# Kernel optimization log

Hardware: AMD Instinct MI355X
Metric: run time of the kernel (lower is better)

The kernel has to match this reference:

```python
import jax, jax.numpy as jnp
import numpy as np

N, K, C_S, C_Z, C_G, N_RBF = 1024, 16, 256, 128, 16, 64
EPS = 1e-8


def _ln(x, g, b, eps=1e-5):
    m = x.mean(-1, keepdims=True)
    v = jnp.mean((x - m) ** 2, -1, keepdims=True)
    return (x - m) * jax.lax.rsqrt(v + eps) * g + b


def _rbf(D, D_count=N_RBF, D_min=0.0, D_max=20.0):
    mu = jnp.linspace(D_min, D_max, D_count, dtype=D.dtype)
    sigma = (D_max - D_min) / D_count
    return jnp.exp(-(((D[..., None] - mu) / sigma) ** 2))


def setup_inputs() -> dict:
    key = jax.random.key(0)
    ks = jax.random.split(key, 20)
    node_features = jax.random.normal(ks[0], (N, C_S), jnp.float32)
    trans = jax.random.normal(ks[1], (N, 3), jnp.float32) * 5.0  # CA translations, Angstrom-ish
    edge_features = jax.random.normal(ks[2], (N * K, C_Z), jnp.float32)
    # sparse graph laid out as K neighbors per node: dst = node i repeated K times
    src = jax.random.randint(ks[3], (N * K,), 0, N)
    dst = jnp.repeat(jnp.arange(N), K)
    edge_index = jnp.stack([src, dst]).astype(jnp.int64)
    batch = jnp.zeros((N,), jnp.int64)
    res_mask = jnp.ones((N,), bool)
    w = lambda k, i, o: jax.random.normal(k, (i, o), jnp.float32) * 0.02
    return {
        "node_features": node_features, "trans": trans, "edge_features": edge_features,
        "ln_g": jnp.ones((C_Z,), jnp.float32), "ln_b": jnp.zeros((C_Z,), jnp.float32),
        "Wl": w(ks[4], C_S, C_G), "bl": jnp.zeros((C_G,), jnp.float32),
        "Wr": w(ks[5], C_S, C_G), "br": jnp.zeros((C_G,), jnp.float32),
        "Wep": w(ks[6], C_Z, C_Z), "bep": jnp.zeros((C_Z,), jnp.float32),
        "Weg": w(ks[7], C_Z, C_Z), "beg": jnp.zeros((C_Z,), jnp.float32),
        "Wdg": w(ks[8], C_G * C_G, C_Z), "bdg": jnp.zeros((C_Z,), jnp.float32),
        "Wdp": w(ks[9], N_RBF, C_Z), "bdp": jnp.zeros((C_Z,), jnp.float32),
        "lno_g": jnp.ones((C_Z,), jnp.float32), "lno_b": jnp.zeros((C_Z,), jnp.float32),
        "Wout": w(ks[10], C_Z, C_Z), "bout": jnp.zeros((C_Z,), jnp.float32),
        "Wog": w(ks[11], C_Z, C_Z), "bog": jnp.zeros((C_Z,), jnp.float32),
        "edge_index": edge_index, "batch": batch, "res_mask": res_mask,
    }


def reference(node_features, trans, edge_features, ln_g, ln_b, Wl, bl, Wr, br,
              Wep, bep, Weg, beg, Wdg, bdg, Wdp, bdp, lno_g, lno_b, Wout, bout,
              Wog, bog, edge_index, batch, res_mask):
    n = node_features.shape[0]
    src = edge_index[0].reshape(n, K)              # neighbor indices per node [N,K]
    # sparse -> kNN: edges are grouped K per destination node
    knn_feats = edge_features.reshape(n, K, C_Z)
    knn_mask = res_mask[src] & res_mask[:, None]   # [N,K]
    z = _ln(knn_feats, ln_g, ln_b)
    # outer-product node gating
    nl = node_features @ Wl + bl                   # [N,c_g]
    nr = node_features @ Wr + br
    a = nl[src]                                    # [N,K,c_g]
    b = nr[src]
    edge3 = a[:, :, None, :, None] * b[:, None, :, None, :]   # [N,K,K,c_g,c_g]
    gate3 = edge3.reshape(n, K, K, C_G * C_G) @ Wdg + bdg     # [N,K,K,c_z]
    # RBF distance features among the K neighbors of each node
    t = trans[src]                                 # [N,K,3]
    d = jnp.linalg.norm(t[:, :, None, :] - t[:, None, :, :] + EPS, axis=-1)  # [N,K,K]
    df = _rbf(d) @ Wdp + bdp                       # [N,K,K,c_z]
    m2 = (knn_mask[:, :, None] & knn_mask[:, None, :]).astype(df.dtype)
    e3 = jax.nn.sigmoid(gate3) * df * m2[..., None]
    # gated edge projection
    e2 = jax.nn.sigmoid(z @ Weg + beg) * (z @ Wep + bep)      # [N,K,c_z]
    # triangle matmul: per channel c, [K,K] @ [K]
    upd = jnp.einsum('njkc,nkc->njc', e3, e2)                 # [N,K,c_z]
    upd = _ln(upd, lno_g, lno_b) @ Wout + bout
    upd = upd * jax.nn.sigmoid(z @ Wog + bog)
    # kNN -> sparse scatter back (masked)
    out = (upd * knn_mask[..., None].astype(upd.dtype)).reshape(n * K, C_Z)
    return out
```

## Files before the change

### kernel.cpp

```cpp
#include <hip/hip_runtime.h>
#include <math.h>

#define KNN  16
#define CZ   128
#define CG   16
#define CS   256
#define NN   1024

typedef __attribute__((ext_vector_type(8))) _Float16 half8;
typedef __attribute__((ext_vector_type(4))) _Float16 half4;
typedef __attribute__((ext_vector_type(2))) _Float16 half2v;
typedef __attribute__((ext_vector_type(4))) float f4_t;

#define MFMA16x32(A, B, C) __builtin_amdgcn_mfma_f32_16x16x32_f16((A), (B), (C), 0, 0, 0)
#define MFMA16x16(A, B, C) __builtin_amdgcn_mfma_f32_16x16x16f16((A), (B), (C), 0, 0, 0)

union U8 { half2v h[4]; half8 v; };
union U4 { half2v h[2]; half4 v; };

__device__ __forceinline__ half2v pk2(float x, float y) {
    auto t = __builtin_amdgcn_cvt_pkrtz(x, y);
    half2v r;
    __builtin_memcpy(&r, &t, 4);
    return r;
}
__device__ __forceinline__ float sig_(float x) {
    return __builtin_amdgcn_rcpf(1.0f + __expf(-x));
}

__global__ __launch_bounds__(256) void prep_kernel(
    const float* __restrict__ Wdp, const float* __restrict__ Wdg,
    const float* __restrict__ Wout, const float* __restrict__ Wep,
    const float* __restrict__ Weg, const float* __restrict__ Wog,
    _Float16* __restrict__ pk,
    const float* __restrict__ nf,
    const float* __restrict__ Wl, const float* __restrict__ bl,
    const float* __restrict__ Wr, const float* __restrict__ br,
    float* __restrict__ nlo, float* __restrict__ nro) {
    __shared__ float pl[4][16], pr[4][16];
    int b = blockIdx.x, tid = threadIdx.x;
    if (b < 416) {
        int gid = b * 256 + tid;
        float val;
        if (gid >= 8192 && gid < 40960) {
            int o = gid - 8192;
            int i = o & 3, l = (o >> 2) & 63, ct = (o >> 8) & 7, q = o >> 11;
            int row = (4 * (l >> 4) + i) * 16 + q;
            int col = ct * 16 + (l & 15);
            val = Wdg[row * CZ + col];
        } else {
            const float* srcw;
            int o;
            if (gid < 8192)        { srcw = Wdp;  o = gid; }
            else if (gid < 57344)  { srcw = Wout; o = gid - 40960; }
            else if (gid < 73728)  { srcw = Wep;  o = gid - 57344; }
            else if (gid < 90112)  { srcw = Weg;  o = gid - 73728; }
            else                   { srcw = Wog;  o = gid - 90112; }
            int t = o & 7, l = (o >> 3) & 63, ct = (o >> 9) & 7, s = o >> 12;
            int row = s * 32 + (l >> 4) * 8 + t;
            int col = ct * 16 + (l & 15);
            val = srcw[row * CZ + col];
        }
        pk[gid] = (_Float16)val;
    } else {
        int n = b - 416;
        int wv = tid >> 6, lane = tid & 63;
        int p = lane & 15, sub = lane >> 4;
        int base = wv * 64 + sub * 16;
        const float* rw = nf + n * CS + base;
        const float* wlp = Wl + base * CG + p;
        const float* wrp = Wr + base * CG + p;
        float accl = 0.0f, accr = 0.0f;
        #pragma unroll
        for (int i = 0; i < 16; ++i) {
            float v = rw[i];
            accl += v * wlp[i * CG];
            accr += v * wrp[i * CG];
        }
        accl += __shfl_xor(accl, 16); accl += __shfl_xor(accl, 32);
        accr += __shfl_xor(accr, 16); accr += __shfl_xor(accr, 32);
        if (lane < 16) { pl[wv][lane] = accl; pr[wv][lane] = accr; }
        __syncthreads();
        if (tid < 16) {
            nlo[n * CG + tid] = pl[0][tid] + pl[1][tid] + pl[2][tid] + pl[3][tid] + bl[tid];
        } else if (tid < 32) {
            int p2 = tid - 16;
            nro[n * CG + p2] = pr[0][p2] + pr[1][p2] + pr[2][p2] + pr[3][p2] + br[p2];
        }
    }
}

__global__ __launch_bounds__(256) void main_kernel(
    const float* __restrict__ trans, const float* __restrict__ ef,
    const float* __restrict__ lng, const float* __restrict__ lnb,
    const float* __restrict__ nl, const float* __restrict__ nr,
    const float* __restrict__ bep, const float* __restrict__ beg,
    const float* __restrict__ bog,
    const _Float16* __restrict__ Wepp, const _Float16* __restrict__ Wegp,
    const _Float16* __restrict__ Wogp,
    const _Float16* __restrict__ Wdg2, const float* __restrict__ bdg,
    const _Float16* __restrict__ Wdpp, const float* __restrict__ bdp,
    const float* __restrict__ lnog, const float* __restrict__ lnob,
    const _Float16* __restrict__ Woutp, const float* __restrict__ bout,
    const int* __restrict__ src, const int* __restrict__ resmask,
    float* __restrict__ out) {
    __shared__ _Float16 s_zu[16 * 136];
    __shared__ float s_t[64];
    __shared__ float s_km[16];
    __shared__ int   s_src[16];
    __shared__ float s_a[256];
    __shared__ float s_b[16 * 20];
    __shared__ _Float16 s_T[4 * 2048];
    __shared__ _Float16 s_fr[8 * 64 * 8];
    __shared__ _Float16 s_part[16 * CZ * 4];

    int n = blockIdx.x, tid = threadIdx.x;
    if (tid < 16) {
        int sv = src[n * KNN + tid];
        s_src[tid] = sv;
        s_km[tid] = (resmask[sv] != 0 && resmask[n] != 0) ? 1.0f : 0.0f;
        s_t[tid * 4 + 0] = trans[sv * 3 + 0];
        s_t[tid * 4 + 1] = trans[sv * 3 + 1];
        s_t[tid * 4 + 2] = trans[sv * 3 + 2];
    }
    __syncthreads();
    {
        int j = tid >> 4, p = tid & 15;
        int sv = s_src[j];
        s_a[j * 16 + p] = nl[sv * CG + p];
        s_b[j * 20 + p] = nr[sv * CG + p];
    }
    {
        int r = tid >> 4, seg = tid & 15;
        const float* row = ef + ((size_t)n * KNN + r) * CZ + seg * 8;
        f4_t x0 = *(const f4_t*)row;
        f4_t x1 = *(const f4_t*)(row + 4);
        float s = x0.x + x0.y + x0.z + x0.w + x1.x + x1.y + x1.z + x1.w;
        float q = x0.x * x0.x + x0.y * x0.y + x0.z * x0.z + x0.w * x0.w
                + x1.x * x1.x + x1.y * x1.y + x1.z * x1.z + x1.w * x1.w;
        #pragma unroll
        for (int m = 1; m < 16; m <<= 1) { s += __shfl_xor(s, m); q += __shfl_xor(q, m); }
        float mean = s * (1.0f / CZ);
        float var  = q * (1.0f / CZ) - mean * mean;
        float rs   = __builtin_amdgcn_rsqf(var + 1e-5f);
        int col = seg * 8;
        f4_t g0 = *(const f4_t*)(lng + col), g1 = *(const f4_t*)(lng + col + 4);
        f4_t b0 = *(const f4_t*)(lnb + col), b1 = *(const f4_t*)(lnb + col + 4);
        U8 zu;
        zu.h[0] = pk2((x0.x - mean) * rs * g0.x + b0.x, (x0.y - mean) * rs * g0.y + b0.y);
        zu.h[1] = pk2((x0.z - mean) * rs * g0.z + b0.z, (x0.w - mean) * rs * g0.w + b0.w);
        zu.h[2] = pk2((x1.x - mean) * rs * g1.x + b1.x, (x1.y - mean) * rs * g1.y + b1.y);
        zu.h[3] = pk2((x1.z - mean) * rs * g1.z + b1.z, (x1.w - mean) * rs * g1.w + b1.w);
        *(half8*)&s_zu[r * 136 + col] = zu.v;
    }
    __syncthreads();

    int wv = tid >> 6, lane = tid & 63, l15 = lane & 15, quad = lane >> 4;

    half8 Az[4];
    #pragma unroll
    for (int st = 0; st < 4; ++st)
        Az[st] = *(const half8*)&s_zu[l15 * 136 + st * 32 + quad * 8];
    f4_t e2f[2], ggf[2];
    #pragma unroll
    for (int cc = 0; cc < 2; ++cc) {
        int ct = wv * 2 + cc;
        int c = ct * 16 + l15;
        float vep = bep[c], veg = beg[c], vog = bog[c];
        f4_t aep = {vep, vep, vep, vep};
        f4_t aeg = {veg, veg, veg, veg};
        f4_t aog = {vog, vog, vog, vog};
        #pragma unroll
        for (int st = 0; st < 4; ++st) {
            int off = ((st * 8 + ct) * 64 + lane) * 8;
            half8 wep_ = *(const half8*)(Wepp + off);
            half8 weg_ = *(const half8*)(Wegp + off);
            half8 wog_ = *(const half8*)(Wogp + off);
            aep = MFMA16x32(Az[st], wep_, aep);
            aeg = MFMA16x32(Az[st], weg_, aeg);
            aog = MFMA16x32(Az[st], wog_, aog);
        }
        #pragma unroll
        for (int rr = 0; rr < 4; ++rr) {
            e2f[cc][rr] = sig_(aeg[rr]) * aep[rr] * s_km[quad * 4 + rr];
            ggf[cc][rr] = sig_(aog[rr]);
        }
    }
    __syncthreads();

    {
        U8 g;
        g.h[0] = pk2(ggf[0][0], ggf[0][1]);
        g.h[1] = pk2(ggf[0][2], ggf[0][3]);
        g.h[2] = pk2(ggf[1][0], ggf[1][1]);
        g.h[3] = pk2(ggf[1][2], ggf[1][3]);
        *(half8*)&s_zu[tid * 8] = g.v;
    }

    half8 Bdp_[2][2];
    #pragma unroll
    for (int st = 0; st < 2; ++st)
        #pragma unroll
        for (int cc = 0; cc < 2; ++cc)
            Bdp_[st][cc] = *(const half8*)(Wdpp + ((st * 8 + wv * 2 + cc) * 64 + lane) * 8);

    float bdgv[2], bdpv[2];
    #pragma unroll
    for (int cc = 0; cc < 2; ++cc) {
        int c = (wv * 2 + cc) * 16 + l15;
        bdgv[cc] = bdg[c];
        bdpv[cc] = bdp[c];
    }

    half4 Aa, Ab;
    {
        f4_t av = *(const f4_t*)&s_a[l15 * 16 + 4 * quad];
        U4 u; u.h[0] = pk2(av.x, av.y); u.h[1] = pk2(av.z, av.w);
        Aa = u.v;
        f4_t bv = *(const f4_t*)&s_b[l15 * 20 + 4 * quad];
        U4 w; w.h[0] = pk2(bv.x, bv.y); w.h[1] = pk2(bv.z, bv.w);
        Ab = w.v;
    }

    float tkx = s_t[l15 * 4 + 0], tky = s_t[l15 * 4 + 1], tkz = s_t[l15 * 4 + 2];
    const float MUS = 20.0f / 63.0f;
    const float ISG = 1.0f / 0.3125f;
    float rIS[2];
    #pragma unroll
    for (int st = 0; st < 2; ++st)
        rIS[st] = (float)(st * 32 + quad * 8) * (MUS * ISG);

    _Float16* Tw = s_T + wv * 2048;

    for (int Q = 0; Q < 4; ++Q) {
        #pragma unroll
        for (int ctl = 0; ctl < 2; ++ctl) {
            int ct = wv * 2 + ctl;
            #pragma unroll
            for (int qb = 0; qb < 4; ++qb) {
                f4_t tq[4];
                #pragma unroll
                for (int qq = 0; qq < 4; ++qq) {
                    half4 Bw = *(const half4*)(Wdg2 + (((4 * qb + qq) * 8 + ct) * 64 + lane) * 4);
                    f4_t z = {0.f, 0.f, 0.f, 0.f};
                    tq[qq] = MFMA16x16(Aa, Bw, z);
                }
                if (quad == Q) {
                    #pragma unroll
                    for (int rr = 0; rr < 4; ++rr) {
                        U4 u;
                        u.h[0] = pk2(tq[0][rr], tq[1][rr]);
                        u.h[1] = pk2(tq[2][rr], tq[3][rr]);
                        *(half4*)&Tw[((rr * 2 + ctl) * 64 + l15 + 16 * qb) * 4] = u.v;
                    }
                }
            }
        }

        #pragma unroll
        for (int uu = 0; uu < 2; ++uu) {
            int u = wv * 2 + uu;
            int m = u >> 1, st = u & 1;
            int j = 4 * Q + m;
            float dx = s_t[j * 4 + 0] - tkx + 1e-8f;
            float dy = s_t[j * 4 + 1] - tky + 1e-8f;
            float dz = s_t[j * 4 + 2] - tkz + 1e-8f;
            float dI = sqrtf(dx * dx + dy * dy + dz * dz) * ISG;
            float base0 = dI - rIS[st];
            U8 cv;
            #pragma unroll
            for (int tt = 0; tt < 4; ++tt) {
                float u0 = base0 - (float)(2 * tt) * (MUS * ISG);
                float u1 = u0 - (MUS * ISG);
                cv.h[tt] = pk2(__expf(-u0 * u0), __expf(-u1 * u1));
            }
            *(half8*)&s_fr[(u * 64 + lane) * 8] = cv.v;
        }
        __syncthreads();

        for (int m = 0; m < 4; ++m) {
            int j = 4 * Q + m;
            half8 ar0 = *(const half8*)&s_fr[((m * 2 + 0) * 64 + lane) * 8];
            half8 ar1 = *(const half8*)&s_fr[((m * 2 + 1) * 64 + lane) * 8];
            f4_t accd[2], accg[2];
            #pragma unroll
            for (int cc = 0; cc < 2; ++cc) {
                f4_t z = {bdpv[cc], bdpv[cc], bdpv[cc], bdpv[cc]};
                z = MFMA16x32(ar0, Bdp_[0][cc], z);
                z = MFMA16x32(ar1, Bdp_[1][cc], z);
                accd[cc] = z;
                half4 Bt = *(const half4*)&Tw[((m * 2 + cc) * 64 + l15 + 16 * quad) * 4];
                f4_t g = {bdgv[cc], bdgv[cc], bdgv[cc], bdgv[cc]};
                accg[cc] = MFMA16x16(Ab, Bt, g);
            }
            #pragma unroll
            for (int cc = 0; cc < 2; ++cc) {
                float pr = 0.f;
                #pragma unroll
                for (int rr = 0; rr < 4; ++rr)
                    pr += sig_(accg[cc][rr]) * accd[cc][rr] * e2f[cc][rr];
                s_part[(j * CZ + (wv * 2 + cc) * 16 + l15) * 4 + quad] = (_Float16)pr;
            }
        }
        __syncthreads();
    }

    half8 gv = *(const half8*)&s_zu[tid * 8];
    __syncthreads();

    #pragma unroll
    for (int rr2 = 0; rr2 < 4; ++rr2) {
        int rj = wv * 4 + rr2;
        U4 p0, p1;
        p0.v = *(const half4*)&s_part[(rj * CZ + lane) * 4];
        p1.v = *(const half4*)&s_part[(rj * CZ + lane + 64) * 4];
        half2v t0 = p0.h[0] + p0.h[1];
        half2v t1 = p1.h[0] + p1.h[1];
        float x0 = (float)t0[0] + (float)t0[1];
        float x1 = (float)t1[0] + (float)t1[1];
        float sm = x0 + x1, sq = x0 * x0 + x1 * x1;
        #pragma unroll
        for (int m = 1; m < 64; m <<= 1) {
            sm += __shfl_xor(sm, m);
            sq += __shfl_xor(sq, m);
        }
        float mean = sm * (1.0f / CZ);
        float var  = sq * (1.0f / CZ) - mean * mean;
        float rsv  = __builtin_amdgcn_rsqf(var + 1e-5f);
        float h0 = (x0 - mean) * rsv * lnog[lane] + lnob[lane];
        float h1 = (x1 - mean) * rsv * lnog[64 + lane] + lnob[64 + lane];
        s_zu[rj * 136 + lane]      = (_Float16)h0;
        s_zu[rj * 136 + 64 + lane] = (_Float16)h1;
    }
    __syncthreads();

    half8 Aw[4];
    #pragma unroll
    for (int st = 0; st < 4; ++st)
        Aw[st] = *(const half8*)&s_zu[l15 * 136 + st * 32 + quad * 8];
    #pragma unroll
    for (int cc = 0; cc < 2; ++cc) {
        int ct = wv * 2 + cc;
        int c = ct * 16 + l15;
        float bo = bout[c];
        f4_t acc = {bo, bo, bo, bo};
        #pragma unroll
        for (int st = 0; st < 4; ++st) {
            half8 bw = *(const half8*)(Woutp + ((st * 8 + ct) * 64 + lane) * 8);
            acc = MFMA16x32(Aw[st], bw, acc);
        }
        #pragma unroll
        for (int rr = 0; rr < 4; ++rr) {
            int row = quad * 4 + rr;
            size_t oi = (size_t)(n * KNN + row) * CZ + c;
            out[oi] = acc[rr] * (float)gv[cc * 4 + rr] * s_km[row];
        }
    }
}

extern "C" void kernel_launch(void* const* d_in, const int* in_sizes, int n_in,
                              void* d_out, int out_size, void* d_ws, size_t ws_size,
                              hipStream_t stream) {
    const float* node_features = (const float*)d_in[0];
    const float* trans         = (const float*)d_in[1];
    const float* edge_features = (const float*)d_in[2];
    const float* ln_g  = (const float*)d_in[3];
    const float* ln_b  = (const float*)d_in[4];
    const float* Wl    = (const float*)d_in[5];
    const float* bl    = (const float*)d_in[6];
    const float* Wr    = (const float*)d_in[7];
    const float* br    = (const float*)d_in[8];
    const float* Wep   = (const float*)d_in[9];
    const float* bep   = (const float*)d_in[10];
    const float* Weg   = (const float*)d_in[11];
    const float* beg   = (const float*)d_in[12];
    const float* Wdg   = (const float*)d_in[13];
    const float* bdg   = (const float*)d_in[14];
    const float* Wdp   = (const float*)d_in[15];
    const float* bdp   = (const float*)d_in[16];
    const float* lno_g = (const float*)d_in[17];
    const float* lno_b = (const float*)d_in[18];
    const float* Wout  = (const float*)d_in[19];
    const float* bout  = (const float*)d_in[20];
    const float* Wog   = (const float*)d_in[21];
    const float* bog   = (const float*)d_in[22];
    const int* edge_index = (const int*)d_in[23];
    const int* resmask    = (const int*)d_in[25];

    float* ws = (float*)d_ws;
    float* nl = ws;
    float* nr = nl + NN * CG;
    _Float16* pk = (_Float16*)(nr + NN * CG);
    _Float16* Wdpp  = pk;
    _Float16* Wdg2  = pk + 8192;
    _Float16* Woutp = pk + 40960;
    _Float16* Wepp  = pk + 57344;
    _Float16* Wegp  = pk + 73728;
    _Float16* Wogp  = pk + 90112;
    const int* src = edge_index;

    prep_kernel<<<1440, 256, 0, stream>>>(
        Wdp, Wdg, Wout, Wep, Weg, Wog, pk,
        node_features, Wl, bl, Wr, br, nl, nr);
    main_kernel<<<NN, 256, 0, stream>>>(
        trans, edge_features, ln_g, ln_b, nl, nr,
        bep, beg, bog, Wepp, Wegp, Wogp,
        Wdg2, bdg, Wdpp, bdp, lno_g, lno_b,
        Woutp, bout, src, resmask, (float*)d_out);
}
```

Baseline: 150.4 us.

## Double main kernel block to 512 threads, one channel tile per wave

Main kernel now runs 8 waves per block instead of 4, with each wave handling a single 16-channel tile rather than two. The layernorm load, RBF feature generation, triangle partial products and output projection are all re-split across the larger block, and the per-wave shared T buffer is halved. The aim is more parallelism and latency hiding per node at the cost of fewer registers per thread and more threads sharing the same barriers.

```diff
diff --git a/kernel.cpp b/kernel.cpp
--- a/kernel.cpp
+++ b/kernel.cpp
@@ -90,7 +90,7 @@
     }
 }
 
-__global__ __launch_bounds__(256) void main_kernel(
+__global__ __launch_bounds__(512) void main_kernel(
     const float* __restrict__ trans, const float* __restrict__ ef,
     const float* __restrict__ lng, const float* __restrict__ lnb,
     const float* __restrict__ nl, const float* __restrict__ nr,
@@ -110,7 +110,7 @@
     __shared__ int   s_src[16];
     __shared__ float s_a[256];
     __shared__ float s_b[16 * 20];
-    __shared__ _Float16 s_T[4 * 2048];
+    __shared__ _Float16 s_T[8 * 1024];
     __shared__ _Float16 s_fr[8 * 64 * 8];
     __shared__ _Float16 s_part[16 * CZ * 4];
 
@@ -124,48 +124,43 @@
         s_t[tid * 4 + 2] = trans[sv * 3 + 2];
     }
     __syncthreads();
-    {
+    if (tid < 256) {
         int j = tid >> 4, p = tid & 15;
         int sv = s_src[j];
         s_a[j * 16 + p] = nl[sv * CG + p];
         s_b[j * 20 + p] = nr[sv * CG + p];
     }
     {
-        int r = tid >> 4, seg = tid & 15;
-        const float* row = ef + ((size_t)n * KNN + r) * CZ + seg * 8;
-        f4_t x0 = *(const f4_t*)row;
-        f4_t x1 = *(const f4_t*)(row + 4);
-        float s = x0.x + x0.y + x0.z + x0.w + x1.x + x1.y + x1.z + x1.w;
-        float q = x0.x * x0.x + x0.y * x0.y + x0.z * x0.z + x0.w * x0.w
-                + x1.x * x1.x + x1.y * x1.y + x1.z * x1.z + x1.w * x1.w;
-        #pragma unroll
-        for (int m = 1; m < 16; m <<= 1) { s += __shfl_xor(s, m); q += __shfl_xor(q, m); }
+        int r = tid >> 5, seg = tid & 31;
+        int col = seg * 4;
+        const float* row = ef + ((size_t)n * KNN + r) * CZ + col;
+        f4_t x = *(const f4_t*)row;
+        float s = x.x + x.y + x.z + x.w;
+        float q = x.x * x.x + x.y * x.y + x.z * x.z + x.w * x.w;
+        #pragma unroll
+        for (int m = 1; m < 32; m <<= 1) { s += __shfl_xor(s, m); q += __shfl_xor(q, m); }
         float mean = s * (1.0f / CZ);
         float var  = q * (1.0f / CZ) - mean * mean;
         float rs   = __builtin_amdgcn_rsqf(var + 1e-5f);
-        int col = seg * 8;
-        f4_t g0 = *(const f4_t*)(lng + col), g1 = *(const f4_t*)(lng + col + 4);
-        f4_t b0 = *(const f4_t*)(lnb + col), b1 = *(const f4_t*)(lnb + col + 4);
-        U8 zu;
-        zu.h[0] = pk2((x0.x - mean) * rs * g0.x + b0.x, (x0.y - mean) * rs * g0.y + b0.y);
-        zu.h[1] = pk2((x0.z - mean) * rs * g0.z + b0.z, (x0.w - mean) * rs * g0.w + b0.w);
-        zu.h[2] = pk2((x1.x - mean) * rs * g1.x + b1.x, (x1.y - mean) * rs * g1.y + b1.y);
-        zu.h[3] = pk2((x1.z - mean) * rs * g1.z + b1.z, (x1.w - mean) * rs * g1.w + b1.w);
-        *(half8*)&s_zu[r * 136 + col] = zu.v;
+        f4_t g = *(const f4_t*)(lng + col);
+        f4_t bb = *(const f4_t*)(lnb + col);
+        U4 zu;
+        zu.h[0] = pk2((x.x - mean) * rs * g.x + bb.x, (x.y - mean) * rs * g.y + bb.y);
+        zu.h[1] = pk2((x.z - mean) * rs * g.z + bb.z, (x.w - mean) * rs * g.w + bb.w);
+        *(half4*)&s_zu[r * 136 + col] = zu.v;
     }
     __syncthreads();
 
     int wv = tid >> 6, lane = tid & 63, l15 = lane & 15, quad = lane >> 4;
+    int ct = wv;
+    int c = ct * 16 + l15;
 
     half8 Az[4];
     #pragma unroll
     for (int st = 0; st < 4; ++st)
         Az[st] = *(const half8*)&s_zu[l15 * 136 + st * 32 + quad * 8];
-    f4_t e2f[2], ggf[2];
-    #pragma unroll
-    for (int cc = 0; cc < 2; ++cc) {
-        int ct = wv * 2 + cc;
-        int c = ct * 16 + l15;
+    f4_t e2f, ggf;
+    {
         float vep = bep[c], veg = beg[c], vog = bog[c];
         f4_t aep = {vep, vep, vep, vep};
         f4_t aeg = {veg, veg, veg, veg};
@@ -182,35 +177,25 @@
         }
         #pragma unroll
         for (int rr = 0; rr < 4; ++rr) {
-            e2f[cc][rr] = sig_(aeg[rr]) * aep[rr] * s_km[quad * 4 + rr];
-            ggf[cc][rr] = sig_(aog[rr]);
-        }
-    }
-    __syncthreads();
-
-    {
-        U8 g;
-        g.h[0] = pk2(ggf[0][0], ggf[0][1]);
-        g.h[1] = pk2(ggf[0][2], ggf[0][3]);
-        g.h[2] = pk2(ggf[1][0], ggf[1][1]);
-        g.h[3] = pk2(ggf[1][2], ggf[1][3]);
-        *(half8*)&s_zu[tid * 8] = g.v;
-    }
-
-    half8 Bdp_[2][2];
+            e2f[rr] = sig_(aeg[rr]) * aep[rr] * s_km[quad * 4 + rr];
+            ggf[rr] = sig_(aog[rr]);
+        }
+    }
+    __syncthreads();
+
+    {
+        U4 g;
+        g.h[0] = pk2(ggf[0], ggf[1]);
+        g.h[1] = pk2(ggf[2], ggf[3]);
+        *(half4*)&s_zu[tid * 4] = g.v;
+    }
+
+    half8 Bdp_[2];
     #pragma unroll
     for (int st = 0; st < 2; ++st)
-        #pragma unroll
-        for (int cc = 0; cc < 2; ++cc)
-            Bdp_[st][cc] = *(const half8*)(Wdpp + ((st * 8 + wv * 2 + cc) * 64 + lane) * 8);
-
-    float bdgv[2], bdpv[2];
-    #pragma unroll
-    for (int cc = 0; cc < 2; ++cc) {
-        int c = (wv * 2 + cc) * 16 + l15;
-        bdgv[cc] = bdg[c];
-        bdpv[cc] = bdp[c];
-    }
+        Bdp_[st] = *(const half8*)(Wdpp + ((st * 8 + ct) * 64 + lane) * 8);
+
+    float bdgv = bdg[c], bdpv = bdp[c];
 
     half4 Aa, Ab;
     {
@@ -225,48 +210,39 @@
     float tkx = s_t[l15 * 4 + 0], tky = s_t[l15 * 4 + 1], tkz = s_t[l15 * 4 + 2];
     const float MUS = 20.0f / 63.0f;
     const float ISG = 1.0f / 0.3125f;
-    float rIS[2];
-    #pragma unroll
-    for (int st = 0; st < 2; ++st)
-        rIS[st] = (float)(st * 32 + quad * 8) * (MUS * ISG);
-
-    _Float16* Tw = s_T + wv * 2048;
+    int ust = wv & 1;
+    float rISu = (float)(ust * 32 + quad * 8) * (MUS * ISG);
+
+    _Float16* Tw = s_T + wv * 1024;
 
     for (int Q = 0; Q < 4; ++Q) {
         #pragma unroll
-        for (int ctl = 0; ctl < 2; ++ctl) {
-            int ct = wv * 2 + ctl;
+        for (int qb = 0; qb < 4; ++qb) {
+            f4_t tq[4];
             #pragma unroll
-            for (int qb = 0; qb < 4; ++qb) {
-                f4_t tq[4];
+            for (int qq = 0; qq < 4; ++qq) {
+                half4 Bw = *(const half4*)(Wdg2 + (((4 * qb + qq) * 8 + ct) * 64 + lane) * 4);
+                f4_t z = {0.f, 0.f, 0.f, 0.f};
+                tq[qq] = MFMA16x16(Aa, Bw, z);
+            }
+            if (quad == Q) {
                 #pragma unroll
-                for (int qq = 0; qq < 4; ++qq) {
-                    half4 Bw = *(const half4*)(Wdg2 + (((4 * qb + qq) * 8 + ct) * 64 + lane) * 4);
-                    f4_t z = {0.f, 0.f, 0.f, 0.f};
-                    tq[qq] = MFMA16x16(Aa, Bw, z);
-                }
-                if (quad == Q) {
-                    #pragma unroll
-                    for (int rr = 0; rr < 4; ++rr) {
-                        U4 u;
-                        u.h[0] = pk2(tq[0][rr], tq[1][rr]);
-                        u.h[1] = pk2(tq[2][rr], tq[3][rr]);
-                        *(half4*)&Tw[((rr * 2 + ctl) * 64 + l15 + 16 * qb) * 4] = u.v;
-                    }
+                for (int rr = 0; rr < 4; ++rr) {
+                    U4 u;
+                    u.h[0] = pk2(tq[0][rr], tq[1][rr]);
+                    u.h[1] = pk2(tq[2][rr], tq[3][rr]);
+                    *(half4*)&Tw[(rr * 64 + l15 + 16 * qb) * 4] = u.v;
                 }
             }
         }
 
-        #pragma unroll
-        for (int uu = 0; uu < 2; ++uu) {
-            int u = wv * 2 + uu;
-            int m = u >> 1, st = u & 1;
-            int j = 4 * Q + m;
+        {
+            int j = 4 * Q + (wv >> 1);
             float dx = s_t[j * 4 + 0] - tkx + 1e-8f;
             float dy = s_t[j * 4 + 1] - tky + 1e-8f;
             float dz = s_t[j * 4 + 2] - tkz + 1e-8f;
             float dI = sqrtf(dx * dx + dy * dy + dz * dz) * ISG;
-            float base0 = dI - rIS[st];
+            float base0 = dI - rISu;
             U8 cv;
             #pragma unroll
             for (int tt = 0; tt < 4; ++tt) {
@@ -274,7 +250,7 @@
                 float u1 = u0 - (MUS * ISG);
                 cv.h[tt] = pk2(__expf(-u0 * u0), __expf(-u1 * u1));
             }
-            *(half8*)&s_fr[(u * 64 + lane) * 8] = cv.v;
+            *(half8*)&s_fr[(wv * 64 + lane) * 8] = cv.v;
         }
         __syncthreads();
 
@@ -282,35 +258,27 @@
             int j = 4 * Q + m;
             half8 ar0 = *(const half8*)&s_fr[((m * 2 + 0) * 64 + lane) * 8];
             half8 ar1 = *(const half8*)&s_fr[((m * 2 + 1) * 64 + lane) * 8];
-            f4_t accd[2], accg[2];
+            f4_t accd = {bdpv, bdpv, bdpv, bdpv};
+            accd = MFMA16x32(ar0, Bdp_[0], accd);
+            accd = MFMA16x32(ar1, Bdp_[1], accd);
+            half4 Bt = *(const half4*)&Tw[(m * 64 + l15 + 16 * quad) * 4];
+            f4_t accg = {bdgv, bdgv, bdgv, bdgv};
+            accg = MFMA16x16(Ab, Bt, accg);
+            float pr = 0.f;
             #pragma unroll
-            for (int cc = 0; cc < 2; ++cc) {
-                f4_t z = {bdpv[cc], bdpv[cc], bdpv[cc], bdpv[cc]};
-                z = MFMA16x32(ar0, Bdp_[0][cc], z);
-                z = MFMA16x32(ar1, Bdp_[1][cc], z);
-                accd[cc] = z;
-                half4 Bt = *(const half4*)&Tw[((m * 2 + cc) * 64 + l15 + 16 * quad) * 4];
-                f4_t g = {bdgv[cc], bdgv[cc], bdgv[cc], bdgv[cc]};
-                accg[cc] = MFMA16x16(Ab, Bt, g);
-            }
-            #pragma unroll
-            for (int cc = 0; cc < 2; ++cc) {
-                float pr = 0.f;
-                #pragma unroll
-                for (int rr = 0; rr < 4; ++rr)
-                    pr += sig_(accg[cc][rr]) * accd[cc][rr] * e2f[cc][rr];
-                s_part[(j * CZ + (wv * 2 + cc) * 16 + l15) * 4 + quad] = (_Float16)pr;
-            }
+            for (int rr = 0; rr < 4; ++rr)
+                pr += sig_(accg[rr]) * accd[rr] * e2f[rr];
+            s_part[(j * CZ + c) * 4 + quad] = (_Float16)pr;
         }
         __syncthreads();
     }
 
-    half8 gv = *(const half8*)&s_zu[tid * 8];
+    half4 gv = *(const half4*)&s_zu[tid * 4];
     __syncthreads();
 
     #pragma unroll
-    for (int rr2 = 0; rr2 < 4; ++rr2) {
-        int rj = wv * 4 + rr2;
+    for (int rr2 = 0; rr2 < 2; ++rr2) {
+        int rj = wv * 2 + rr2;
         U4 p0, p1;
         p0.v = *(const half4*)&s_part[(rj * CZ + lane) * 4];
         p1.v = *(const half4*)&s_part[(rj * CZ + lane + 64) * 4];
@@ -338,10 +306,7 @@
     #pragma unroll
     for (int st = 0; st < 4; ++st)
         Aw[st] = *(const half8*)&s_zu[l15 * 136 + st * 32 + quad * 8];
-    #pragma unroll
-    for (int cc = 0; cc < 2; ++cc) {
-        int ct = wv * 2 + cc;
-        int c = ct * 16 + l15;
+    {
         float bo = bout[c];
         f4_t acc = {bo, bo, bo, bo};
         #pragma unroll
@@ -353,7 +318,7 @@
         for (int rr = 0; rr < 4; ++rr) {
             int row = quad * 4 + rr;
             size_t oi = (size_t)(n * KNN + row) * CZ + c;
-            out[oi] = acc[rr] * (float)gv[cc * 4 + rr] * s_km[row];
+            out[oi] = acc[rr] * (float)gv[rr] * s_km[row];
         }
     }
 }
@@ -402,7 +367,7 @@
     prep_kernel<<<1440, 256, 0, stream>>>(
         Wdp, Wdg, Wout, Wep, Weg, Wog, pk,
         node_features, Wl, bl, Wr, br, nl, nr);
-    main_kernel<<<NN, 256, 0, stream>>>(
+    main_kernel<<<NN, 512, 0, stream>>>(
         trans, edge_features, ln_g, ln_b, nl, nr,
         bep, beg, bog, Wepp, Wegp, Wogp,
         Wdg2, bdg, Wdpp, bdp, lno_g, lno_b,
```

Measured after the change: 148.3 us. About the same (-1.4%).
